# Kernel optimization log

Measured on AMD Instinct MI355X. Metric: run time of the kernel, lower is better.

The kernel has to match this reference:

```python
import jax, jax.numpy as jnp
import numpy as np

B, NX, NC, D, H = 4, 1024, 154, 1536, 24
HD = D // H
MH = int(D * 4.0)
EPS = 1e-6


def setup_inputs() -> dict:
    key = jax.random.key(0)
    ks = jax.random.split(key, 20)
    s = lambda i, shape, fan: jax.random.normal(ks[i], shape, jnp.float32) * (1.0 / np.sqrt(fan))
    return {
        "x": jax.random.normal(ks[0], (B, NX, D), jnp.float32),
        "c": jax.random.normal(ks[1], (B, NC, D), jnp.float32),
        "vec": jax.random.normal(ks[2], (B, D), jnp.float32),
        "w_mod": s(3, (D, 6 * D), D), "b_mod": jnp.zeros((6 * D,), jnp.float32),
        "w_qkv_x": s(4, (D, 3 * D), D), "b_qkv_x": jnp.zeros((3 * D,), jnp.float32),
        "w_qkv_c": s(5, (D, 3 * D), D), "b_qkv_c": jnp.zeros((3 * D,), jnp.float32),
        "w_proj_x": s(6, (D, D), D), "b_proj_x": jnp.zeros((D,), jnp.float32),
        "w_proj_c": s(7, (D, D), D), "b_proj_c": jnp.zeros((D,), jnp.float32),
        "w1_x": s(8, (D, MH), D), "b1_x": jnp.zeros((MH,), jnp.float32),
        "w2_x": s(9, (MH, D), MH), "b2_x": jnp.zeros((D,), jnp.float32),
        "w1_c": s(10, (D, MH), D), "b1_c": jnp.zeros((MH,), jnp.float32),
        "w2_c": s(11, (MH, D), MH), "b2_c": jnp.zeros((D,), jnp.float32),
    }


def _ln(t):
    m = jnp.mean(t, axis=-1, keepdims=True)
    v = jnp.var(t, axis=-1, keepdims=True)
    return (t - m) * jax.lax.rsqrt(v + EPS)


def reference(x, c, vec, w_mod, b_mod, w_qkv_x, b_qkv_x, w_qkv_c, b_qkv_c,
              w_proj_x, b_proj_x, w_proj_c, b_proj_c,
              w1_x, b1_x, w2_x, b2_x, w1_c, b1_c, w2_c, b2_c):
    # adaLN modulation: silu(vec) @ W -> 6 chunks, each [B,1,D]
    mod = (jax.nn.silu(vec) @ w_mod + b_mod)[:, None, :]
    sh_x, sc_x, g_x, sh_c, sc_c, g_c = jnp.split(mod, 6, axis=2)

    x_n = _ln(x) * (1 + sc_x) + sh_x
    c_n = _ln(c) * (1 + sc_c) + sh_c

    def qkv(t, w, b, n):
        o = (t @ w + b).reshape(t.shape[0], n, 3, H, HD)
        return o[:, :, 0], o[:, :, 1], o[:, :, 2]  # each [B,N,H,HD]

    qx, kx, vx = qkv(x_n, w_qkv_x, b_qkv_x, NX)
    qc, kc, vc = qkv(c_n, w_qkv_c, b_qkv_c, NC)
    q = jnp.concatenate([qx, qc], axis=1)
    k = jnp.concatenate([kx, kc], axis=1)
    v = jnp.concatenate([vx, vc], axis=1)

    scale = HD ** -0.5
    attn = jnp.einsum("bshd,bthd->bhst", q, k) * scale
    attn = jax.nn.softmax(attn, axis=-1)
    o = jnp.einsum("bhst,bthd->bshd", attn, v).reshape(B, NX + NC, D)
    xo, co = o[:, :NX], o[:, NX:]

    x = x + g_x * (xo @ w_proj_x + b_proj_x)
    c = c + g_c * (co @ w_proj_c + b_proj_c)

    gelu = lambda t: jax.nn.gelu(t, approximate=True)
    x = x + (gelu(_ln(x) @ w1_x + b1_x) @ w2_x + b2_x)
    c = c + (gelu(_ln(c) @ w1_c + b1_c) @ w2_c + b2_c)
    return x, c
```

## Files before the change

### kernel.cpp

```cpp
#include <hip/hip_runtime.h>
#include <stdint.h>

typedef unsigned short u16;
typedef unsigned int u32;
typedef __attribute__((ext_vector_type(8))) short bf16x8;
typedef __attribute__((ext_vector_type(8))) unsigned short u16x8;
typedef __attribute__((ext_vector_type(2))) unsigned int u32x2;
typedef __attribute__((ext_vector_type(4))) float f32x4;

#define LB256 __launch_bounds__(256, 2)

#define BB 4
#define NX 1024
#define NC 154
#define NT 1178
#define NTP 1184
#define DD 1536
#define HH 24
#define MHD 6144
#define NQKV 4608
#define NMOD 9216
#define KSPL 6

__device__ __forceinline__ int imin(int a, int b) { return a < b ? a : b; }

__device__ __forceinline__ u16 f2bf(float f) {
  u32 u = __float_as_uint(f);
  u32 r = (u + 0x7fffu + ((u >> 16) & 1u)) >> 16;
  return (u16)r;
}

__device__ __forceinline__ float bf2f(u16 v) {
  u32 u = ((u32)v) << 16;
  return __uint_as_float(u);
}

__device__ __forceinline__ float gelu_t(float x) {
  float u = 1.5957691216f * x * fmaf(0.044715f, x * x, 1.f);
  return x / (1.f + __expf(-u));
}

__device__ __forceinline__ f32x4 fzero4() {
  f32x4 z; z[0] = 0.f; z[1] = 0.f; z[2] = 0.f; z[3] = 0.f; return z;
}

__device__ __forceinline__ void glds16(const u16* g, u16* l) {
  __builtin_amdgcn_global_load_lds(
      (const __attribute__((address_space(1))) void*)g,
      (__attribute__((address_space(3))) void*)l, 16, 0, 0);
}

#define WAITV0 asm volatile("s_waitcnt vmcnt(0)" ::: "memory")
#define SCHEDB __builtin_amdgcn_sched_barrier(0)

struct TDesc {
  const float* W[8];
  u16* Wt[8];
  int K[8];
  int N[8];
  int off[9];
};

__global__ void k_transpose8(TDesc d) {
  __shared__ float tile[32][33];
  int bid = blockIdx.x;
  int i = 0;
#pragma unroll
  for (int t = 1; t < 8; ++t)
    if (bid >= d.off[t]) i = t;
  const float* W = d.W[i];
  u16* Wt = d.Wt[i];
  const int K = d.K[i], N = d.N[i];
  const int local = bid - d.off[i];
  const int nbx = N >> 5;
  const int n0 = (local % nbx) * 32, k0 = (local / nbx) * 32;
  const int cx = threadIdx.x & 15, ry = threadIdx.x >> 4;
#pragma unroll
  for (int j = 0; j < 32; j += 16) {
    float2 t2 = *(const float2*)&W[(size_t)(k0 + ry + j) * N + n0 + cx * 2];
    tile[ry + j][cx * 2] = t2.x;
    tile[ry + j][cx * 2 + 1] = t2.y;
  }
  __syncthreads();
#pragma unroll
  for (int j = 0; j < 32; j += 16) {
    const int ny = ry + j;
    u32 w = (u32)f2bf(tile[cx * 2][ny]) | ((u32)f2bf(tile[cx * 2 + 1][ny]) << 16);
    *(u32*)&Wt[(size_t)(n0 + ny) * K + k0 + cx * 2] = w;
  }
}

__global__ void k_mod_part(const float* __restrict__ vec, const float* __restrict__ w_mod,
                           float* __restrict__ part) {
  __shared__ float sv[BB][256];
  int n = blockIdx.x * 256 + threadIdx.x;
  int kb = blockIdx.y;
  int k0 = kb * 256;
  for (int i = threadIdx.x; i < BB * 256; i += 256) {
    int b = i >> 8, kk = i & 255;
    float v = vec[b * DD + k0 + kk];
    sv[b][kk] = v / (1.f + __expf(-v));
  }
  __syncthreads();
  float a0 = 0.f, a1 = 0.f, a2 = 0.f, a3 = 0.f;
  for (int k = 0; k < 256; ++k) {
    float w = w_mod[(size_t)(k0 + k) * NMOD + n];
    a0 = fmaf(sv[0][k], w, a0);
    a1 = fmaf(sv[1][k], w, a1);
    a2 = fmaf(sv[2][k], w, a2);
    a3 = fmaf(sv[3][k], w, a3);
  }
  part[((size_t)kb * BB + 0) * NMOD + n] = a0;
  part[((size_t)kb * BB + 1) * NMOD + n] = a1;
  part[((size_t)kb * BB + 2) * NMOD + n] = a2;
  part[((size_t)kb * BB + 3) * NMOD + n] = a3;
}

__global__ void k_mod_red(const float* __restrict__ part, const float* __restrict__ b_mod,
                          float* __restrict__ mod) {
  int n = blockIdx.x * 256 + threadIdx.x;
  float bb = b_mod[n];
#pragma unroll
  for (int b = 0; b < BB; ++b) {
    float s = bb;
#pragma unroll
    for (int kb = 0; kb < KSPL; ++kb) s += part[((size_t)kb * BB + b) * NMOD + n];
    mod[b * NMOD + n] = s;
  }
}

__global__ LB256 void k_ln2(const float* __restrict__ in1, u16* __restrict__ out1,
                            const float* __restrict__ in2, u16* __restrict__ out2,
                            const float* __restrict__ modp, int sh1, int sc1,
                            int sh2, int sc2) {
  int row = blockIdx.x;
  const float* xr;
  u16* outp;
  int b, sh, sc;
  if (row < BB * NX) {
    xr = in1 + (size_t)row * DD;
    outp = out1 + (size_t)row * DD;
    b = row / NX; sh = sh1; sc = sc1;
  } else {
    int r2 = row - BB * NX;
    xr = in2 + (size_t)r2 * DD;
    outp = out2 + (size_t)r2 * DD;
    b = r2 / NC; sh = sh2; sc = sc2;
  }
  const float2* x2p = (const float2*)xr;
  float2 v[3];
  float s = 0.f, s2 = 0.f;
#pragma unroll
  for (int i = 0; i < 3; ++i) {
    float2 t = x2p[threadIdx.x + 256 * i];
    v[i] = t;
    s += t.x + t.y;
    s2 += t.x * t.x + t.y * t.y;
  }
#pragma unroll
  for (int m = 32; m >= 1; m >>= 1) {
    s += __shfl_xor(s, m);
    s2 += __shfl_xor(s2, m);
  }
  __shared__ float red[8];
  int wid = threadIdx.x >> 6;
  if ((threadIdx.x & 63) == 0) { red[wid] = s; red[4 + wid] = s2; }
  __syncthreads();
  s = red[0] + red[1] + red[2] + red[3];
  s2 = red[4] + red[5] + red[6] + red[7];
  float mean = s * (1.f / (float)DD);
  float var = s2 * (1.f / (float)DD) - mean * mean;
  float rstd = rsqrtf(var + 1e-6f);
#pragma unroll
  for (int i = 0; i < 3; ++i) {
    int d = (threadIdx.x + 256 * i) * 2;
    float y0 = (v[i].x - mean) * rstd;
    float y1 = (v[i].y - mean) * rstd;
    if (modp) {
      float2 scv = *(const float2*)&modp[b * NMOD + sc + d];
      float2 shv = *(const float2*)&modp[b * NMOD + sh + d];
      y0 = y0 * (1.f + scv.x) + shv.x;
      y1 = y1 * (1.f + scv.y) + shv.y;
    }
    u32 w = (u32)f2bf(y0) | ((u32)f2bf(y1) << 16);
    *(u32*)&outp[d] = w;
  }
}

template <int EPI>
__device__ __forceinline__ void gemm_epi(
    const f32x4 (&acc)[4][4], int m0, int n0, int wm, int wn, int g, int r,
    int M, int N, const float* bias, void* outp, const float* resid,
    const float* modp, int goff, int rpb, int zed,
    u16* qb, u16* kb, u16* vtb) {
#pragma unroll
  for (int mi = 0; mi < 4; ++mi) {
#pragma unroll
    for (int ni = 0; ni < 4; ++ni) {
      const int col = n0 + wn + ni * 16 + r;
      float bv = 0.f;
      if constexpr (EPI != 4) bv = bias[col];
#pragma unroll
      for (int j = 0; j < 4; ++j) {
        const int row = m0 + wm + mi * 16 + g * 4 + j;
        if (row >= M) continue;
        const size_t off = (size_t)row * N + col;
        float v = acc[mi][ni][j] + bv;
        if constexpr (EPI == 0) {
          ((u16*)outp)[off] = f2bf(v);
        } else if constexpr (EPI == 1) {
          ((u16*)outp)[off] = f2bf(gelu_t(v));
        } else if constexpr (EPI == 2) {
          const int b = row / rpb;
          ((float*)outp)[off] = resid[off] + modp[b * NMOD + goff + col] * v;
        } else if constexpr (EPI == 3) {
          ((float*)outp)[off] = resid[off] + v;
        } else if constexpr (EPI == 4) {
          ((u16*)outp)[(size_t)zed * (size_t)goff + off] = f2bf(acc[mi][ni][j]);
        } else {
          const int b = row / rpb;
          const int t = goff + (row - b * rpb);
          const u16 bw = f2bf(v);
          if (col < DD) {
            const int h = col >> 6, d = col & 63;
            qb[(((size_t)b * HH + h) * NT + t) * 64 + d] = bw;
          } else if (col < 2 * DD) {
            const int cc = col - DD;
            const int h = cc >> 6, d = cc & 63;
            kb[(((size_t)b * HH + h) * NT + t) * 64 + d] = bw;
          } else {
            const int cc = col - 2 * DD;
            const int h = cc >> 6, d = cc & 63;
            vtb[((size_t)b * HH + h) * (64 * NTP) + (size_t)d * NTP + t] = bw;
          }
        }
      }
    }
  }
}

template <int EPI1, int EPI2>
__global__ LB256 void k_gemm2(
    const u16* __restrict__ A1, const u16* __restrict__ Bt1, const float* __restrict__ bias1,
    int M1, int rpb1, int goff1, int kLen1,
    const u16* __restrict__ A2, const u16* __restrict__ Bt2, const float* __restrict__ bias2,
    int M2, int rpb2, int goff2, int kLen2,
    int yHi, int N, int lda, int ldb, int kzOff,
    void* __restrict__ out1, void* __restrict__ out2,
    const float* __restrict__ resid1, const float* __restrict__ resid2,
    const float* __restrict__ modp,
    u16* __restrict__ qb, u16* __restrict__ kb, u16* __restrict__ vtb) {
  __shared__ __align__(16) u16 sm[2 * 8192];
  const int tid = threadIdx.x;
  const int lane = tid & 63;
  const int g = lane >> 4, r = lane & 15;
  const int wid = tid >> 6;

  const int gx = gridDim.x;
  const int gyTot = gridDim.y;
  const int nwg = gx * gyTot;
  int wg = blockIdx.y * gx + blockIdx.x;
  {
    int q = nwg >> 3, rr = nwg & 7;
    int xcd = wg & 7, sl = wg >> 3;
    wg = (xcd < rr ? xcd * (q + 1) : rr * (q + 1) + (xcd - rr) * q) + sl;
  }
  int mIdx, nIdx;
  {
    const int np1 = (gx - 1) >> 3;
    const int lastw = gx - np1 * 8;
    const int full = gyTot * 8;
    if (wg < np1 * full) {
      int p = wg / full, off = wg % full;
      mIdx = off >> 3;
      nIdx = p * 8 + (off & 7);
    } else {
      int off = wg - np1 * full;
      mIdx = off / lastw;
      nIdx = np1 * 8 + off % lastw;
    }
  }
  const bool role2 = mIdx >= yHi;

  const u16* A = role2 ? A2 : A1;
  const u16* Bt = role2 ? Bt2 : Bt1;
  const int M = role2 ? M2 : M1;
  const int kLen = role2 ? kLen2 : kLen1;
  const int m0 = (role2 ? (mIdx - yHi) : mIdx) * 128, n0 = nIdx * 128;
  const int wm = (wid >> 1) * 64, wn = (wid & 1) * 64;
  A += (size_t)blockIdx.z * kzOff;
  Bt += (size_t)blockIdx.z * kzOff;

  f32x4 acc[4][4];
#pragma unroll
  for (int i = 0; i < 4; ++i)
#pragma unroll
    for (int j = 0; j < 4; ++j) acc[i][j] = fzero4();

  const int rl = lane >> 2;
  const int slg = (lane & 3) ^ ((lane >> 3) & 3);
  const int c0 = wid * 2, c1 = wid * 2 + 1;
  const size_t aR0 = (size_t)imin(m0 + c0 * 16 + rl, M - 1) * lda + slg * 8;
  const size_t aR1 = (size_t)imin(m0 + c1 * 16 + rl, M - 1) * lda + slg * 8;
  const size_t bR0 = (size_t)(n0 + c0 * 16 + rl) * ldb + slg * 8;
  const size_t bR1 = (size_t)(n0 + c1 * 16 + rl) * ldb + slg * 8;

  int aOff[4], bOff[4];
#pragma unroll
  for (int mi = 0; mi < 4; ++mi) aOff[mi] = (wm + mi * 16 + r) * 32 + ((g ^ ((r >> 1) & 3)) * 8);
#pragma unroll
  for (int ni = 0; ni < 4; ++ni) bOff[ni] = 4096 + (wn + ni * 16 + r) * 32 + ((g ^ ((r >> 1) & 3)) * 8);

  const int nt = kLen >> 5;

#define STAGE32(BI, T)                                      \
  do {                                                      \
    u16* bb = &sm[(BI) * 8192];                             \
    size_t kk = (size_t)(T) * 32;                           \
    glds16(A + aR0 + kk, bb + c0 * 512);                    \
    glds16(A + aR1 + kk, bb + c1 * 512);                    \
    glds16(Bt + bR0 + kk, bb + 4096 + c0 * 512);            \
    glds16(Bt + bR1 + kk, bb + 4096 + c1 * 512);            \
  } while (0)

  STAGE32(0, 0);

  for (int t = 0; t < nt; ++t) {
    WAITV0;
    __builtin_amdgcn_s_barrier();
    SCHEDB;
    if (t + 1 < nt) STAGE32((t + 1) & 1, t + 1);
    const u16* bb = &sm[(t & 1) * 8192];
    bf16x8 af[4], bfr[4];
#pragma unroll
    for (int mi = 0; mi < 4; ++mi) af[mi] = *(const bf16x8*)(bb + aOff[mi]);
#pragma unroll
    for (int ni = 0; ni < 4; ++ni) bfr[ni] = *(const bf16x8*)(bb + bOff[ni]);
    __builtin_amdgcn_s_setprio(1);
#pragma unroll
    for (int mi = 0; mi < 4; ++mi)
#pragma unroll
      for (int ni = 0; ni < 4; ++ni)
        acc[mi][ni] = __builtin_amdgcn_mfma_f32_16x16x32_bf16(af[mi], bfr[ni], acc[mi][ni], 0, 0, 0);
    __builtin_amdgcn_s_setprio(0);
    SCHEDB;
  }
#undef STAGE32

  if (role2)
    gemm_epi<EPI2>(acc, m0, n0, wm, wn, g, r, M, N, bias2, out2, resid2, modp,
                   goff2, rpb2, blockIdx.z, qb, kb, vtb);
  else
    gemm_epi<EPI1>(acc, m0, n0, wm, wn, g, r, M, N, bias1, out1, resid1, modp,
                   goff1, rpb1, blockIdx.z, qb, kb, vtb);
}

__global__ void k_red2(const u16* __restrict__ p0x, const u16* __restrict__ p1x,
                       const float* __restrict__ residx, const float* __restrict__ bx,
                       const u16* __restrict__ p0c, const u16* __restrict__ p1c,
                       const float* __restrict__ residc, const float* __restrict__ bc,
                       float* __restrict__ outx, float* __restrict__ outc) {
  int row = blockIdx.x;
  if (row < BB * NX) {
    size_t base = (size_t)row * DD;
#pragma unroll
    for (int i = 0; i < 6; ++i) {
      int j = threadIdx.x + 256 * i;
      outx[base + j] = residx[base + j] + bx[j] + bf2f(p0x[base + j]) + bf2f(p1x[base + j]);
    }
  } else {
    size_t base = (size_t)(row - BB * NX) * DD;
#pragma unroll
    for (int i = 0; i < 6; ++i) {
      int j = threadIdx.x + 256 * i;
      outc[base + j] = residc[base + j] + bc[j] + bf2f(p0c[base + j]) + bf2f(p1c[base + j]);
    }
  }
}

__global__ __launch_bounds__(512, 2) void k_attn(
    const u16* __restrict__ q, const u16* __restrict__ kk,
    const u16* __restrict__ vt, u16* __restrict__ ox, u16* __restrict__ oc) {
  __shared__ __align__(16) u16 Ks[64][72];
  __shared__ __align__(16) u16 Vs[64][72];
  __shared__ __align__(16) u16 Ps[8][16][72];

  const int lane = threadIdx.x & 63, wid = threadIdx.x >> 6;
  const int g = lane >> 4, r = lane & 15;
  const int q0 = blockIdx.x * 128;
  const int h = blockIdx.y, b = blockIdx.z;
  const size_t bh = (size_t)b * HH + h;
  const u16* qp = q + bh * (NT * 64);
  const u16* kp = kk + bh * (NT * 64);
  const u16* vp = vt + bh * (64 * NTP);

  const int qrow = imin(q0 + wid * 16 + r, NT - 1);
  u16x8 qr0 = *(const u16x8*)(qp + (size_t)qrow * 64 + g * 8);
  u16x8 qr1 = *(const u16x8*)(qp + (size_t)qrow * 64 + 32 + g * 8);
  bf16x8 qa0, qa1;
#pragma unroll
  for (int e = 0; e < 8; ++e) {
    qa0[e] = (short)f2bf(bf2f(qr0[e]) * 0.125f);
    qa1[e] = (short)f2bf(bf2f(qr1[e]) * 0.125f);
  }

  f32x4 oacc[4];
#pragma unroll
  for (int i = 0; i < 4; ++i) oacc[i] = fzero4();
  float mrow = -1e30f, lrow = 0.f;

  const int trA = threadIdx.x >> 3;
  const int ccA = (threadIdx.x & 7) * 8;

  u16x8 kreg, vreg;
#define LOADKV(T0)                                                     \
  do {                                                                 \
    int tsrc = imin((T0) + trA, NT - 1);                               \
    kreg = *(const u16x8*)(kp + (size_t)tsrc * 64 + ccA);              \
    int tcol = (T0) + ccA;                                             \
    if (tcol + 8 <= NT) {                                              \
      vreg = *(const u16x8*)(vp + (size_t)trA * NTP + tcol);           \
    } else {                                                           \
      _Pragma("unroll")                                                \
      for (int e = 0; e < 8; ++e)                                      \
        vreg[e] = vp[(size_t)trA * NTP + imin(tcol + e, NT - 1)];      \
    }                                                                  \
  } while (0)

  LOADKV(0);

  for (int t0 = 0; t0 < NT; t0 += 64) {
    if (t0) __syncthreads();
    *(u16x8*)&Ks[trA][ccA] = kreg;
    *(u16x8*)&Vs[trA][ccA] = vreg;
    __syncthreads();
    if (t0 + 64 < NT) LOADKV(t0 + 64);

    f32x4 s[4];
#pragma unroll
    for (int ni = 0; ni < 4; ++ni) {
      s[ni] = fzero4();
      s[ni] = __builtin_amdgcn_mfma_f32_16x16x32_bf16(*(const bf16x8*)&Ks[ni * 16 + r][g * 8], qa0, s[ni], 0, 0, 0);
      s[ni] = __builtin_amdgcn_mfma_f32_16x16x32_bf16(*(const bf16x8*)&Ks[ni * 16 + r][32 + g * 8], qa1, s[ni], 0, 0, 0);
    }

    float pv[4][4];
    float pm = -1e30f;
#pragma unroll
    for (int ni = 0; ni < 4; ++ni)
#pragma unroll
      for (int j = 0; j < 4; ++j) {
        int t = t0 + ni * 16 + g * 4 + j;
        float sv = (t < NT) ? s[ni][j] : -1e30f;
        pv[ni][j] = sv;
        pm = fmaxf(pm, sv);
      }
    pm = fmaxf(pm, __shfl_xor(pm, 16));
    pm = fmaxf(pm, __shfl_xor(pm, 32));

    float mn = fmaxf(mrow, pm);
    float alpha = __expf(mrow - mn);
    mrow = mn;
    float rs = 0.f;
#pragma unroll
    for (int ni = 0; ni < 4; ++ni)
#pragma unroll
      for (int j = 0; j < 4; ++j) {
        float p = __expf(pv[ni][j] - mn);
        pv[ni][j] = p;
        rs += p;
      }
    rs += __shfl_xor(rs, 16);
    rs += __shfl_xor(rs, 32);
    lrow = lrow * alpha + rs;

#pragma unroll
    for (int j = 0; j < 4; ++j) {
      float aj = __shfl(alpha, g * 4 + j);
#pragma unroll
      for (int ni = 0; ni < 4; ++ni) oacc[ni][j] *= aj;
    }

#pragma unroll
    for (int ni = 0; ni < 4; ++ni) {
      u32x2 w;
      w[0] = (u32)f2bf(pv[ni][0]) | ((u32)f2bf(pv[ni][1]) << 16);
      w[1] = (u32)f2bf(pv[ni][2]) | ((u32)f2bf(pv[ni][3]) << 16);
      *(u32x2*)&Ps[wid][r][ni * 16 + g * 4] = w;
    }

    bf16x8 pa0 = *(const bf16x8*)&Ps[wid][r][g * 8];
    bf16x8 pa1 = *(const bf16x8*)&Ps[wid][r][32 + g * 8];
#pragma unroll
    for (int ni = 0; ni < 4; ++ni) {
      oacc[ni] = __builtin_amdgcn_mfma_f32_16x16x32_bf16(pa0, *(const bf16x8*)&Vs[ni * 16 + r][g * 8], oacc[ni], 0, 0, 0);
      oacc[ni] = __builtin_amdgcn_mfma_f32_16x16x32_bf16(pa1, *(const bf16x8*)&Vs[ni * 16 + r][32 + g * 8], oacc[ni], 0, 0, 0);
    }
  }
#undef LOADKV

  float linv[4];
#pragma unroll
  for (int j = 0; j < 4; ++j) linv[j] = 1.f / __shfl(lrow, g * 4 + j);

#pragma unroll
  for (int ni = 0; ni < 4; ++ni)
#pragma unroll
    for (int j = 0; j < 4; ++j) {
      int tq = q0 + wid * 16 + g * 4 + j;
      if (tq >= NT) continue;
      float val = oacc[ni][j] * linv[j];
      int col = h * 64 + ni * 16 + r;
      if (tq < NX)
        ox[(size_t)(b * NX + tq) * DD + col] = f2bf(val);
      else
        oc[(size_t)(b * NC + tq - NX) * DD + col] = f2bf(val);
    }
}

extern "C" void kernel_launch(void* const* d_in, const int* in_sizes, int n_in,
                              void* d_out, int out_size, void* d_ws, size_t ws_size,
                              hipStream_t stream) {
  const float* x = (const float*)d_in[0];
  const float* c = (const float*)d_in[1];
  const float* vec = (const float*)d_in[2];
  const float* w_mod = (const float*)d_in[3];
  const float* b_mod = (const float*)d_in[4];
  const float* w_qkv_x = (const float*)d_in[5];
  const float* b_qkv_x = (const float*)d_in[6];
  const float* w_qkv_c = (const float*)d_in[7];
  const float* b_qkv_c = (const float*)d_in[8];
  const float* w_proj_x = (const float*)d_in[9];
  const float* b_proj_x = (const float*)d_in[10];
  const float* w_proj_c = (const float*)d_in[11];
  const float* b_proj_c = (const float*)d_in[12];
  const float* w1_x = (const float*)d_in[13];
  const float* b1_x = (const float*)d_in[14];
  const float* w2_x = (const float*)d_in[15];
  const float* b2_x = (const float*)d_in[16];
  const float* w1_c = (const float*)d_in[17];
  const float* b1_c = (const float*)d_in[18];
  const float* w2_c = (const float*)d_in[19];
  const float* b2_c = (const float*)d_in[20];

  if (ws_size < 229195776ull) return;

  char* ws = (char*)d_ws;
  u16* wt_qkv_x = (u16*)(ws + 0);
  u16* wt_qkv_c = (u16*)(ws + 14155776);
  u16* wt_proj_x = (u16*)(ws + 28311552);
  u16* wt_proj_c = (u16*)(ws + 33030144);
  u16* wt_w1_x = (u16*)(ws + 37748736);
  u16* wt_w1_c = (u16*)(ws + 56623104);
  u16* wt_w2_x = (u16*)(ws + 75497472);
  u16* wt_w2_c = (u16*)(ws + 94371840);
  float* modf = (float*)(ws + 113246208);
  char* S = ws + 113393664;
  u16* xn = (u16*)(S);
  u16* cn = (u16*)(S + 12582912);
  float* x2 = (float*)(S + 14475264);
  float* c2 = (float*)(S + 39641088);
  u16* pb0 = (u16*)(S);
  u16* pc0 = (u16*)(S + 12582912);
  u16* pb1 = (u16*)(S + 43425792);
  u16* pc1 = (u16*)(S + 56008704);
  const int PSTRIDE = 43425792 / 2;
  u16* qb = (u16*)(S + 57901056);
  u16* kb = (u16*)(S + 72376320);
  u16* vtb = (u16*)(S + 86851584);
  u16* hx = (u16*)(S + 57901056);
  u16* hc = (u16*)(S + 108232704);
  float* modpart = (float*)(S + 57901056);

  {
    TDesc d;
    const float* Ws[8] = {w_qkv_x, w_qkv_c, w_proj_x, w_proj_c, w1_x, w1_c, w2_x, w2_c};
    u16* Wts[8] = {wt_qkv_x, wt_qkv_c, wt_proj_x, wt_proj_c, wt_w1_x, wt_w1_c, wt_w2_x, wt_w2_c};
    int Ks[8] = {DD, DD, DD, DD, DD, DD, MHD, MHD};
    int Ns[8] = {NQKV, NQKV, DD, DD, MHD, MHD, DD, DD};
    int off = 0;
    for (int i = 0; i < 8; ++i) {
      d.W[i] = Ws[i]; d.Wt[i] = Wts[i]; d.K[i] = Ks[i]; d.N[i] = Ns[i];
      d.off[i] = off;
      off += (Ns[i] >> 5) * (Ks[i] >> 5);
    }
    d.off[8] = off;
    k_transpose8<<<dim3(off), 256, 0, stream>>>(d);
  }

  k_mod_part<<<dim3(NMOD / 256, KSPL), 256, 0, stream>>>(vec, w_mod, modpart);
  k_mod_red<<<dim3(NMOD / 256), 256, 0, stream>>>(modpart, b_mod, modf);

  k_ln2<<<dim3(BB * (NX + NC)), 256, 0, stream>>>(x, xn, c, cn, modf, 0, DD, 3 * DD, 4 * DD);

  k_gemm2<5, 5><<<dim3(NQKV / 128, 37), 256, 0, stream>>>(
      xn, wt_qkv_x, b_qkv_x, BB * NX, NX, 0, DD,
      cn, wt_qkv_c, b_qkv_c, BB * NC, NC, NX, DD,
      32, NQKV, DD, DD, 0, nullptr, nullptr, nullptr, nullptr, nullptr,
      qb, kb, vtb);

  k_attn<<<dim3((NT + 127) / 128, HH, BB), 512, 0, stream>>>(qb, kb, vtb, xn, cn);

  k_gemm2<2, 2><<<dim3(DD / 128, 37), 256, 0, stream>>>(
      xn, wt_proj_x, b_proj_x, BB * NX, NX, 2 * DD, DD,
      cn, wt_proj_c, b_proj_c, BB * NC, NC, 5 * DD, DD,
      32, DD, DD, DD, 0, x2, c2, x, c, modf, nullptr, nullptr, nullptr);

  k_ln2<<<dim3(BB * (NX + NC)), 256, 0, stream>>>(x2, xn, c2, cn, nullptr, 0, 0, 0, 0);

  k_gemm2<1, 1><<<dim3(MHD / 128, 37), 256, 0, stream>>>(
      xn, wt_w1_x, b1_x, BB * NX, NX, 0, DD,
      cn, wt_w1_c, b1_c, BB * NC, NC, 0, DD,
      32, MHD, DD, DD, 0, hx, hc, nullptr, nullptr, nullptr, nullptr, nullptr, nullptr);

  float* outx = (float*)d_out;
  float* outc = outx + (size_t)BB * NX * DD;
  k_gemm2<4, 4><<<dim3(DD / 128, 37, 2), 256, 0, stream>>>(
      hx, wt_w2_x, b2_x, BB * NX, NX, PSTRIDE, MHD / 2,
      hc, wt_w2_c, b2_c, BB * NC, NC, PSTRIDE, MHD / 2,
      32, DD, MHD, MHD, MHD / 2, pb0, pc0, nullptr, nullptr, nullptr,
      nullptr, nullptr, nullptr);
  k_red2<<<dim3(BB * (NX + NC)), 256, 0, stream>>>(
      pb0, pb1, x2, b2_x, pc0, pc1, c2, b2_c, outx, outc);
}
```

Measured before the change: 658.2 us.

## Fold modulation GEMV into transpose launch, vectorize reduction, lazy softmax rescale

The adaLN modulation partial GEMV now runs as extra blocks appended to the weight-transpose kernel, which removes one launch and lets the two overlap. The k_red2 residual reduction is rewritten to use paired u32/float2 loads and stores. In attention, interior K/V tiles take an unclamped load path. The online-softmax rescale of the accumulators is skipped when no row maximum grows in the wave, at the cost of a warp vote and extra divergence logic.

```diff
diff --git a/kernel.cpp b/kernel.cpp
--- a/kernel.cpp
+++ b/kernel.cpp
@@ -59,11 +59,40 @@
   int K[8];
   int N[8];
   int off[9];
+  const float* vec;
+  const float* w_mod;
+  float* part;
 };
 
 __global__ void k_transpose8(TDesc d) {
-  __shared__ float tile[32][33];
+  __shared__ float shf[32 * 33];
   int bid = blockIdx.x;
+  if (bid >= d.off[8]) {
+    float(*sv)[256] = (float(*)[256])shf;
+    const int local = bid - d.off[8];
+    const int kb = local / (NMOD / 256);
+    const int n = (local % (NMOD / 256)) * 256 + threadIdx.x;
+    const int k0 = kb * 256;
+    for (int i = threadIdx.x; i < BB * 256; i += 256) {
+      int b = i >> 8, kk = i & 255;
+      float v = d.vec[b * DD + k0 + kk];
+      sv[b][kk] = v / (1.f + __expf(-v));
+    }
+    __syncthreads();
+    float a0 = 0.f, a1 = 0.f, a2 = 0.f, a3 = 0.f;
+    for (int k = 0; k < 256; ++k) {
+      float w = d.w_mod[(size_t)(k0 + k) * NMOD + n];
+      a0 = fmaf(sv[0][k], w, a0);
+      a1 = fmaf(sv[1][k], w, a1);
+      a2 = fmaf(sv[2][k], w, a2);
+      a3 = fmaf(sv[3][k], w, a3);
+    }
+    d.part[((size_t)kb * BB + 0) * NMOD + n] = a0;
+    d.part[((size_t)kb * BB + 1) * NMOD + n] = a1;
+    d.part[((size_t)kb * BB + 2) * NMOD + n] = a2;
+    d.part[((size_t)kb * BB + 3) * NMOD + n] = a3;
+    return;
+  }
   int i = 0;
 #pragma unroll
   for (int t = 1; t < 8; ++t)
@@ -78,42 +107,16 @@
 #pragma unroll
   for (int j = 0; j < 32; j += 16) {
     float2 t2 = *(const float2*)&W[(size_t)(k0 + ry + j) * N + n0 + cx * 2];
-    tile[ry + j][cx * 2] = t2.x;
-    tile[ry + j][cx * 2 + 1] = t2.y;
+    shf[(ry + j) * 33 + cx * 2] = t2.x;
+    shf[(ry + j) * 33 + cx * 2 + 1] = t2.y;
   }
   __syncthreads();
 #pragma unroll
   for (int j = 0; j < 32; j += 16) {
     const int ny = ry + j;
-    u32 w = (u32)f2bf(tile[cx * 2][ny]) | ((u32)f2bf(tile[cx * 2 + 1][ny]) << 16);
+    u32 w = (u32)f2bf(shf[(cx * 2) * 33 + ny]) | ((u32)f2bf(shf[(cx * 2 + 1) * 33 + ny]) << 16);
     *(u32*)&Wt[(size_t)(n0 + ny) * K + k0 + cx * 2] = w;
   }
-}
-
-__global__ void k_mod_part(const float* __restrict__ vec, const float* __restrict__ w_mod,
-                           float* __restrict__ part) {
-  __shared__ float sv[BB][256];
-  int n = blockIdx.x * 256 + threadIdx.x;
-  int kb = blockIdx.y;
-  int k0 = kb * 256;
-  for (int i = threadIdx.x; i < BB * 256; i += 256) {
-    int b = i >> 8, kk = i & 255;
-    float v = vec[b * DD + k0 + kk];
-    sv[b][kk] = v / (1.f + __expf(-v));
-  }
-  __syncthreads();
-  float a0 = 0.f, a1 = 0.f, a2 = 0.f, a3 = 0.f;
-  for (int k = 0; k < 256; ++k) {
-    float w = w_mod[(size_t)(k0 + k) * NMOD + n];
-    a0 = fmaf(sv[0][k], w, a0);
-    a1 = fmaf(sv[1][k], w, a1);
-    a2 = fmaf(sv[2][k], w, a2);
-    a3 = fmaf(sv[3][k], w, a3);
-  }
-  part[((size_t)kb * BB + 0) * NMOD + n] = a0;
-  part[((size_t)kb * BB + 1) * NMOD + n] = a1;
-  part[((size_t)kb * BB + 2) * NMOD + n] = a2;
-  part[((size_t)kb * BB + 3) * NMOD + n] = a3;
 }
 
 __global__ void k_mod_red(const float* __restrict__ part, const float* __restrict__ b_mod,
@@ -361,20 +364,29 @@
                        const float* __restrict__ residc, const float* __restrict__ bc,
                        float* __restrict__ outx, float* __restrict__ outc) {
   int row = blockIdx.x;
+  const u16 *p0, *p1;
+  const float *resid, *bias;
+  float* out;
+  size_t base;
   if (row < BB * NX) {
-    size_t base = (size_t)row * DD;
-#pragma unroll
-    for (int i = 0; i < 6; ++i) {
-      int j = threadIdx.x + 256 * i;
-      outx[base + j] = residx[base + j] + bx[j] + bf2f(p0x[base + j]) + bf2f(p1x[base + j]);
-    }
+    p0 = p0x; p1 = p1x; resid = residx; bias = bx; out = outx;
+    base = (size_t)row * DD;
   } else {
-    size_t base = (size_t)(row - BB * NX) * DD;
-#pragma unroll
-    for (int i = 0; i < 6; ++i) {
-      int j = threadIdx.x + 256 * i;
-      outc[base + j] = residc[base + j] + bc[j] + bf2f(p0c[base + j]) + bf2f(p1c[base + j]);
-    }
+    int r2 = row - BB * NX;
+    p0 = p0c; p1 = p1c; resid = residc; bias = bc; out = outc;
+    base = (size_t)r2 * DD;
+  }
+#pragma unroll
+  for (int i = 0; i < 3; ++i) {
+    int j2 = (threadIdx.x + 256 * i) * 2;
+    u32 a = *(const u32*)&p0[base + j2];
+    u32 b = *(const u32*)&p1[base + j2];
+    float2 rv = *(const float2*)&resid[base + j2];
+    float2 bv = *(const float2*)&bias[j2];
+    float2 o;
+    o.x = rv.x + bv.x + bf2f((u16)a) + bf2f((u16)b);
+    o.y = rv.y + bv.y + bf2f((u16)(a >> 16)) + bf2f((u16)(b >> 16));
+    *(float2*)&out[base + j2] = o;
   }
 }
 
@@ -413,7 +425,12 @@
   const int ccA = (threadIdx.x & 7) * 8;
 
   u16x8 kreg, vreg;
-#define LOADKV(T0)                                                     \
+#define LOADKV_C(T0)                                                   \
+  do {                                                                 \
+    kreg = *(const u16x8*)(kp + (size_t)((T0) + trA) * 64 + ccA);      \
+    vreg = *(const u16x8*)(vp + (size_t)trA * NTP + (T0) + ccA);       \
+  } while (0)
+#define LOADKV_E(T0)                                                   \
   do {                                                                 \
     int tsrc = imin((T0) + trA, NT - 1);                               \
     kreg = *(const u16x8*)(kp + (size_t)tsrc * 64 + ccA);              \
@@ -427,14 +444,17 @@
     }                                                                  \
   } while (0)
 
-  LOADKV(0);
+  LOADKV_C(0);
 
   for (int t0 = 0; t0 < NT; t0 += 64) {
     if (t0) __syncthreads();
     *(u16x8*)&Ks[trA][ccA] = kreg;
     *(u16x8*)&Vs[trA][ccA] = vreg;
     __syncthreads();
-    if (t0 + 64 < NT) LOADKV(t0 + 64);
+    if (t0 + 64 < NT) {
+      if (t0 + 128 > NT) LOADKV_E(t0 + 64);
+      else LOADKV_C(t0 + 64);
+    }
 
     f32x4 s[4];
 #pragma unroll
@@ -458,9 +478,9 @@
     pm = fmaxf(pm, __shfl_xor(pm, 16));
     pm = fmaxf(pm, __shfl_xor(pm, 32));
 
-    float mn = fmaxf(mrow, pm);
-    float alpha = __expf(mrow - mn);
-    mrow = mn;
+    const bool grow = !__all(pm <= mrow);
+    float mn = mrow;
+    if (grow) mn = fmaxf(mrow, pm);
     float rs = 0.f;
 #pragma unroll
     for (int ni = 0; ni < 4; ++ni)
@@ -472,13 +492,18 @@
       }
     rs += __shfl_xor(rs, 16);
     rs += __shfl_xor(rs, 32);
-    lrow = lrow * alpha + rs;
-
-#pragma unroll
-    for (int j = 0; j < 4; ++j) {
-      float aj = __shfl(alpha, g * 4 + j);
-#pragma unroll
-      for (int ni = 0; ni < 4; ++ni) oacc[ni][j] *= aj;
+    if (grow) {
+      float alpha = __expf(mrow - mn);
+      mrow = mn;
+      lrow = lrow * alpha + rs;
+#pragma unroll
+      for (int j = 0; j < 4; ++j) {
+        float aj = __shfl(alpha, g * 4 + j);
+#pragma unroll
+        for (int ni = 0; ni < 4; ++ni) oacc[ni][j] *= aj;
+      }
+    } else {
+      lrow += rs;
     }
 
 #pragma unroll
@@ -497,7 +522,8 @@
       oacc[ni] = __builtin_amdgcn_mfma_f32_16x16x32_bf16(pa1, *(const bf16x8*)&Vs[ni * 16 + r][32 + g * 8], oacc[ni], 0, 0, 0);
     }
   }
-#undef LOADKV
+#undef LOADKV_C
+#undef LOADKV_E
 
   float linv[4];
 #pragma unroll
@@ -585,10 +611,12 @@
       off += (Ns[i] >> 5) * (Ks[i] >> 5);
     }
     d.off[8] = off;
-    k_transpose8<<<dim3(off), 256, 0, stream>>>(d);
-  }
-
-  k_mod_part<<<dim3(NMOD / 256, KSPL), 256, 0, stream>>>(vec, w_mod, modpart);
+    d.vec = vec;
+    d.w_mod = w_mod;
+    d.part = modpart;
+    k_transpose8<<<dim3(off + (NMOD / 256) * KSPL), 256, 0, stream>>>(d);
+  }
+
   k_mod_red<<<dim3(NMOD / 256), 256, 0, stream>>>(modpart, b_mod, modf);
 
   k_ln2<<<dim3(BB * (NX + NC)), 256, 0, stream>>>(x, xn, c, cn, modf, 0, DD, 3 * DD, 4 * DD);
```

After: 657.2 us. About the same (-0.2%).
